# Performance work log

Hardware: AMD Instinct MI355X
Metric: run time of the kernel (lower is better)

The kernel has to match this reference:

```python
import jax, jax.numpy as jnp
import numpy as np

EPS = 1.0 / 137.0  # fine-structure-constant epsilon used throughout the Yat ops


def yat_dense(x, W, b, alpha):
    # x: [..., C], W: [C, F] -> [..., F]
    dot = jnp.einsum('btc,cf->btf', x, W)
    x_norm = jnp.sum(x * x, axis=-1, keepdims=True)        # [..., 1]
    w_norm = jnp.sum(W * W, axis=0)                         # [F]
    dist = x_norm + w_norm - 2.0 * dot
    y = dot * dot / (dist + EPS)
    y = y + b
    F = W.shape[1]
    scale = (np.sqrt(F) / np.log(1.0 + F)) ** 1.0           # base; alpha exponent applied below
    return y * ((np.float32(np.sqrt(F)) / np.float32(np.log1p(F))) ** alpha)


def setup_inputs() -> dict:
    key = jax.random.key(0)
    ks = jax.random.split(key, 8)
    B, T, C = 4, 1024, 768
    x = jax.random.normal(ks[0], (B, T, C), dtype=jnp.float32)
    mask = jnp.tril(jnp.ones((T, T), dtype=bool))[None, None, :, :]  # causal [1,1,T,T]
    sd = 1.0 / np.sqrt(C)
    W_attn = jax.random.normal(ks[1], (C, 3 * C), dtype=jnp.float32) * sd
    b_attn = jnp.zeros((3 * C,), dtype=jnp.float32)
    alpha_attn = jnp.ones((), dtype=jnp.float32)
    W_proj = jax.random.normal(ks[2], (C, C), dtype=jnp.float32) * sd
    b_proj = jnp.zeros((C,), dtype=jnp.float32)
    alpha_proj = jnp.ones((), dtype=jnp.float32)
    return {"x": x, "mask": mask, "W_attn": W_attn, "b_attn": b_attn,
            "alpha_attn": alpha_attn, "W_proj": W_proj, "b_proj": b_proj,
            "alpha_proj": alpha_proj}


def reference(x, mask, W_attn, b_attn, alpha_attn, W_proj, b_proj, alpha_proj):
    B, T, C = x.shape
    H = 12
    D = C // H  # head_dim
    qkv = yat_dense(x, W_attn, b_attn, alpha_attn)          # [B,T,3C]
    qkv = qkv.reshape(B, T, 3 * H, D)
    q, k, v = jnp.array_split(qkv, 3, axis=2)
    q = jnp.transpose(q, (0, 2, 1, 3))                       # [B,H,T,D]
    k = jnp.transpose(k, (0, 2, 1, 3))
    v = jnp.transpose(v, (0, 2, 1, 3))
    scale = 1.0 / np.float32(np.sqrt(D))
    dot = jnp.einsum('bhid,bhjd->bhij', q, k)                # [B,H,T,T]
    sq_dot = jnp.square(dot * scale)
    q_norm = jnp.sum(jnp.square(q), axis=-1)[..., None]      # [B,H,T,1]
    k_norm = jnp.sum(jnp.square(k), axis=-1)[..., None, :]   # [B,H,1,T]
    sq_dist = q_norm + k_norm - 2.0 * dot * scale
    attn = sq_dot / (sq_dist + EPS)
    attn = jnp.where(mask, attn, jnp.finfo(jnp.float32).min)
    attn = jax.nn.softmax(attn, axis=-1)
    out = jnp.einsum('bhij,bhjd->bhid', attn, v)             # [B,H,T,D]
    out = jnp.transpose(out, (0, 2, 1, 3)).reshape(B, T, C)
    out = yat_dense(out, W_proj, b_proj, alpha_proj)         # [B,T,C]
    return out
```

## Files before the change

kernel.cpp:

```cpp
#include <hip/hip_runtime.h>
#include <math.h>

#define EPS_YAT (1.0f/137.0f)

typedef unsigned short u16;
typedef unsigned int u32;
typedef __attribute__((ext_vector_type(8))) __bf16 bf16x8;
typedef __attribute__((ext_vector_type(4))) float f32x4;

__device__ __forceinline__ float4 ld4(const float* p) { return *(const float4*)p; }

__device__ __forceinline__ u16 bf16_rne(float f) {
    u32 u = __float_as_uint(f);
    u32 r = (u + 0x7fffu + ((u >> 16) & 1u)) >> 16;
    return (u16)r;
}
__device__ __forceinline__ float bf16_f(u16 h) {
    return __uint_as_float(((u32)h) << 16);
}

__device__ __forceinline__ void glds16(const u16* g, u16* s) {
    __builtin_amdgcn_global_load_lds(
        (const __attribute__((address_space(1))) void*)g,
        (__attribute__((address_space(3))) void*)s,
        16, 0, 0);
}

__global__ void colnorm_part2(const float* __restrict__ Wa, const float* __restrict__ Wp,
                              float* __restrict__ pa, float* __restrict__ pp) {
    __shared__ float sm[256];
    const float* W; float* part; int N, colbase;
    if (blockIdx.x < 36) { W = Wa; part = pa; N = 2304; colbase = blockIdx.x * 64; }
    else                 { W = Wp; part = pp; N = 768;  colbase = (blockIdx.x - 36) * 64; }
    const int col = colbase + (threadIdx.x & 63);
    const int q = threadIdx.x >> 6;
    const int k0 = blockIdx.y * 48 + q * 12;
    float s = 0.f;
    for (int k = k0; k < k0 + 12; ++k) {
        float w = W[(size_t)k * N + col];
        s += w * w;
    }
    sm[threadIdx.x] = s;
    __syncthreads();
    if (threadIdx.x < 64)
        part[(size_t)blockIdx.y * N + col] =
            sm[threadIdx.x] + sm[threadIdx.x + 64] + sm[threadIdx.x + 128] + sm[threadIdx.x + 192];
}

__global__ void colnorm_reduce2(const float* __restrict__ pa, const float* __restrict__ pp,
                                float* __restrict__ wa, float* __restrict__ wp,
                                float* __restrict__ an_zero) {
    int gid = blockIdx.x * 256 + threadIdx.x;
    if (gid < 2304) {
        float s = 0.f;
        #pragma unroll
        for (int i = 0; i < 16; ++i) s += pa[(size_t)i * 2304 + gid];
        wa[gid] = s;
    } else if (gid < 3072) {
        int g = gid - 2304;
        float s = 0.f;
        #pragma unroll
        for (int i = 0; i < 16; ++i) s += pp[(size_t)i * 768 + g];
        wp[g] = s;
    }
    int z = gid - 3072;
    if (z >= 0 && z < 4096) an_zero[z] = 0.f;
}

__global__ void split_rownorm(const float* __restrict__ X, u16* __restrict__ Xh,
                              u16* __restrict__ Xl, float* __restrict__ rn) {
    int wave = threadIdx.x >> 6;
    int lane = threadIdx.x & 63;
    int row = blockIdx.x * 4 + wave;
    const float* xr = X + (size_t)row * 768;
    u16* xh = Xh + (size_t)row * 768;
    u16* xl = Xl + (size_t)row * 768;
    float s = 0.f;
    #pragma unroll
    for (int k = lane * 4; k < 768; k += 256) {
        float4 v = ld4(xr + k);
        s += v.x * v.x + v.y * v.y + v.z * v.z + v.w * v.w;
        u16 h0 = bf16_rne(v.x), h1 = bf16_rne(v.y), h2 = bf16_rne(v.z), h3 = bf16_rne(v.w);
        u16 l0 = bf16_rne(v.x - bf16_f(h0));
        u16 l1 = bf16_rne(v.y - bf16_f(h1));
        u16 l2 = bf16_rne(v.z - bf16_f(h2));
        u16 l3 = bf16_rne(v.w - bf16_f(h3));
        uint2 hp, lp;
        hp.x = (u32)h0 | ((u32)h1 << 16); hp.y = (u32)h2 | ((u32)h3 << 16);
        lp.x = (u32)l0 | ((u32)l1 << 16); lp.y = (u32)l2 | ((u32)l3 << 16);
        *(uint2*)(xh + k) = hp;
        *(uint2*)(xl + k) = lp;
    }
    for (int off = 32; off; off >>= 1) s += __shfl_down(s, off);
    if (lane == 0) rn[row] = s;
}

__global__ void split_wt_kernel(const float* __restrict__ W, u16* __restrict__ Th,
                                u16* __restrict__ Tl, int K, int N) {
    __shared__ float tile[64 * 68];
    const int tid = threadIdx.x;
    const int n0 = blockIdx.x << 6;
    const int k0 = blockIdx.y << 6;
    const int rr = tid >> 4;
    const int cc = (tid & 15) << 2;
    #pragma unroll
    for (int s = 0; s < 4; ++s) {
        int k_l = rr + s * 16;
        *(float4*)&tile[k_l * 68 + cc] = ld4(W + (size_t)(k0 + k_l) * N + n0 + cc);
    }
    __syncthreads();
    #pragma unroll
    for (int s = 0; s < 4; ++s) {
        int n_l = rr + s * 16;
        float a0 = tile[(cc + 0) * 68 + n_l];
        float a1 = tile[(cc + 1) * 68 + n_l];
        float a2 = tile[(cc + 2) * 68 + n_l];
        float a3 = tile[(cc + 3) * 68 + n_l];
        u16 h0 = bf16_rne(a0), h1 = bf16_rne(a1), h2 = bf16_rne(a2), h3 = bf16_rne(a3);
        u16 l0 = bf16_rne(a0 - bf16_f(h0));
        u16 l1 = bf16_rne(a1 - bf16_f(h1));
        u16 l2 = bf16_rne(a2 - bf16_f(h2));
        u16 l3 = bf16_rne(a3 - bf16_f(h3));
        uint2 hp, lp;
        hp.x = (u32)h0 | ((u32)h1 << 16); hp.y = (u32)h2 | ((u32)h3 << 16);
        lp.x = (u32)l0 | ((u32)l1 << 16); lp.y = (u32)l2 | ((u32)l3 << 16);
        size_t o = (size_t)(n0 + n_l) * K + k0 + cc;
        *(uint2*)(Th + o) = hp;
        *(uint2*)(Tl + o) = lp;
    }
}

template<int SPLIT, int BIG>
__global__ __launch_bounds__(256, BIG ? 2 : 4)
void yat_gemm_mfma(const u16* __restrict__ Ah, const u16* __restrict__ Al,
                   const u16* __restrict__ Bh, const u16* __restrict__ Bl,
                   const float* __restrict__ bias, const float* __restrict__ xn,
                   const float* __restrict__ wnc, const float* __restrict__ alphap,
                   const float Fdim, float* __restrict__ out,
                   u16* __restrict__ outh, u16* __restrict__ outl,
                   float* __restrict__ qn, float* __restrict__ kn,
                   const int N, const int K) {
    constexpr int TM = BIG ? 128 : 64;
    constexpr int TN = BIG ? 128 : 64;
    constexpr int JN = BIG ? 4 : 1;
    __shared__ __align__(16) u16 lds[(TM + TN) * 64 * 2];
    const int tid = threadIdx.x;
    const int nwg = gridDim.x * gridDim.y;
    const int orig = blockIdx.y * gridDim.x + blockIdx.x;
    const int swz = (orig & 7) * (nwg >> 3) + (orig >> 3);
    const int m0 = (swz / gridDim.x) * TM;
    const int n0 = (swz % gridDim.x) * TN;
    const int w = tid >> 6;
    const int l = tid & 63;
    const int lm = l & 15;
    const int kq = l >> 4;
    const int kq4 = kq << 2;
    const int WM = BIG ? ((w >> 1) << 6) : 0;
    const int WN = BIG ? ((w & 1) << 6) : (w << 4);

    const int lrow = l >> 3;
    const int lchunk = (l & 7) << 3;

    u16* sAh = lds;
    u16* sAl = lds + TM * 64;
    u16* sBh = lds + 2 * TM * 64;
    u16* sBl = lds + 2 * TM * 64 + TN * 64;

    f32x4 acc[4][JN] = {};

    for (int k0 = 0; k0 < K; k0 += 64) {
        __syncthreads();
        #pragma unroll
        for (int c = 0; c < TM / 32; ++c) {
            const int r0w = (TM / 4) * w + 8 * c;
            const size_t go = (size_t)(m0 + r0w + lrow) * K + k0 + lchunk;
            glds16(Ah + go, sAh + r0w * 64);
            glds16(Al + go, sAl + r0w * 64);
        }
        #pragma unroll
        for (int c = 0; c < TN / 32; ++c) {
            const int r0w = (TN / 4) * w + 8 * c;
            const size_t go = (size_t)(n0 + r0w + lrow) * K + k0 + lchunk;
            glds16(Bh + go, sBh + r0w * 64);
            glds16(Bl + go, sBl + r0w * 64);
        }
        __syncthreads();

        #pragma unroll
        for (int kk = 0; kk < 2; ++kk) {
            bf16x8 fah[4], fal[4], fbh[JN], fbl[JN];
            #pragma unroll
            for (int i = 0; i < 4; ++i) {
                const int ra = (WM + i * 16 + lm) * 64 + kk * 32 + (kq << 3);
                fah[i] = *(const bf16x8*)&sAh[ra];
                fal[i] = *(const bf16x8*)&sAl[ra];
            }
            #pragma unroll
            for (int j = 0; j < JN; ++j) {
                const int rb = (WN + j * 16 + lm) * 64 + kk * 32 + (kq << 3);
                fbh[j] = *(const bf16x8*)&sBh[rb];
                fbl[j] = *(const bf16x8*)&sBl[rb];
            }
            #pragma unroll
            for (int i = 0; i < 4; ++i)
                #pragma unroll
                for (int j = 0; j < JN; ++j) {
                    f32x4 c = acc[i][j];
                    c = __builtin_amdgcn_mfma_f32_16x16x32_bf16(fah[i], fbh[j], c, 0, 0, 0);
                    c = __builtin_amdgcn_mfma_f32_16x16x32_bf16(fah[i], fbl[j], c, 0, 0, 0);
                    c = __builtin_amdgcn_mfma_f32_16x16x32_bf16(fal[i], fbh[j], c, 0, 0, 0);
                    acc[i][j] = c;
                }
        }
    }

    const float scale = powf(sqrtf(Fdim) / log1pf(Fdim), *alphap);
    float pp[4][4];
    #pragma unroll
    for (int i = 0; i < 4; ++i) {
        const int mbase = m0 + WM + i * 16 + kq4;
        #pragma unroll
        for (int r = 0; r < 4; ++r) pp[i][r] = 0.f;
        #pragma unroll
        for (int j = 0; j < JN; ++j) {
            const int n = n0 + WN + j * 16 + lm;
            const float w2 = wnc[n];
            const float bv = bias[n];
            #pragma unroll
            for (int r = 0; r < 4; ++r) {
                const int m = mbase + r;
                float d = acc[i][j][r];
                float den = xn[m] + w2 - 2.f * d + EPS_YAT;
                float v = (d * d / den + bv) * scale;
                if constexpr (SPLIT) {
                    u16 hh = bf16_rne(v);
                    outh[(size_t)m * N + n] = hh;
                    outl[(size_t)m * N + n] = bf16_rne(v - bf16_f(hh));
                    pp[i][r] += v * v;
                } else {
                    out[(size_t)m * N + n] = v;
                }
            }
        }
    }

    if constexpr (SPLIT) {
        const int hcol = n0 + WN;
        if (hcol < 1536) {
            #pragma unroll
            for (int i = 0; i < 4; ++i)
                #pragma unroll
                for (int r = 0; r < 4; ++r) {
                    float s = pp[i][r];
                    s += __shfl_xor(s, 1, 16);
                    s += __shfl_xor(s, 2, 16);
                    s += __shfl_xor(s, 4, 16);
                    s += __shfl_xor(s, 8, 16);
                    if (lm == 0) {
                        const int m = m0 + WM + i * 16 + kq4 + r;
                        const int bb = m >> 10, t = m & 1023;
                        if (hcol < 768)
                            qn[(bb * 12 + (hcol >> 6)) * 1024 + t] = s;
                        else
                            kn[(bb * 12 + ((hcol - 768) >> 6)) * 1024 + t] = s;
                    }
                }
        }
    }
}

#define MFMA_B16(a, b, c) __builtin_amdgcn_mfma_f32_16x16x32_bf16(a, b, c, 0, 0, 0)

#define ST_TILE(j) { \
    const int kro = ((j)*16 + lm) * 72 + (kq << 3); \
    bf16x8 kh = *(const bf16x8*)&KPh[kro]; \
    bf16x8 kl = *(const bf16x8*)&KPl[kro]; \
    st##j = MFMA_B16(kh, qh0, st##j); \
    st##j = MFMA_B16(kl, qh0, st##j); \
    st##j = MFMA_B16(kh, ql0, st##j); \
    kh = *(const bf16x8*)&KPh[kro + 32]; \
    kl = *(const bf16x8*)&KPl[kro + 32]; \
    st##j = MFMA_B16(kh, qh1, st##j); \
    st##j = MFMA_B16(kl, qh1, st##j); \
    st##j = MFMA_B16(kh, ql1, st##j); \
}

#define YAT_EL(j, r) { \
    float sv = st##j[r] * 0.125f; \
    float den = qnm + kns[(j)*16 + kq4 + (r)] - 2.f * sv + EPS_YAT; \
    float v = sv * sv / den; \
    if (diag && ((j)*16 + kq4 + (r) > wband + lm)) v = -3e38f; \
    st##j[r] = v; mm = fmaxf(mm, v); }
#define YAT_TILE(j) YAT_EL(j,0) YAT_EL(j,1) YAT_EL(j,2) YAT_EL(j,3)

#define PEXP_TILE(j) { \
    float p0 = __expf(st##j[0] - mnew), p1 = __expf(st##j[1] - mnew); \
    float p2 = __expf(st##j[2] - mnew), p3 = __expf(st##j[3] - mnew); \
    rs += p0 + p1 + p2 + p3; \
    u16 h0 = bf16_rne(p0), h1 = bf16_rne(p1), h2 = bf16_rne(p2), h3 = bf16_rne(p3); \
    uint2 hp; hp.x = (u32)h0 | ((u32)h1 << 16); hp.y = (u32)h2 | ((u32)h3 << 16); \
    *(uint2*)&KPh[pmrow + (j)*16 + kq4] = hp; \
    u16 e0 = bf16_rne(p0 - bf16_f(h0)), e1 = bf16_rne(p1 - bf16_f(h1)); \
    u16 e2 = bf16_rne(p2 - bf16_f(h2)), e3 = bf16_rne(p3 - bf16_f(h3)); \
    uint2 lp; lp.x = (u32)e0 | ((u32)e1 << 16); lp.y = (u32)e2 | ((u32)e3 << 16); \
    *(uint2*)&KPl[pmrow + (j)*16 + kq4] = lp; }

#define PV_TILE(j) { \
    const int vro = ((j)*16 + lm) * 72 + vkq8; \
    bf16x8 vh = *(const bf16x8*)&Vth[vro]; \
    bf16x8 vl = *(const bf16x8*)&Vtl[vro]; \
    ac##j = MFMA_B16(ph0, vh, ac##j); \
    ac##j = MFMA_B16(pl0, vh, ac##j); \
    ac##j = MFMA_B16(ph0, vl, ac##j); \
    vh = *(const bf16x8*)&Vth[vro + 32]; \
    vl = *(const bf16x8*)&Vtl[vro + 32]; \
    ac##j = MFMA_B16(ph1, vh, ac##j); \
    ac##j = MFMA_B16(pl1, vh, ac##j); \
    ac##j = MFMA_B16(ph1, vl, ac##j); \
}

#define WRVT(dst, v2, m) { \
    dst[(sj * 4 + 16 * (m) + 0) * 72 + toks] = (u16)((v2).x); \
    dst[(sj * 4 + 16 * (m) + 1) * 72 + toks] = (u16)((v2).x >> 16); \
    dst[(sj * 4 + 16 * (m) + 2) * 72 + toks] = (u16)((v2).y); \
    dst[(sj * 4 + 16 * (m) + 3) * 72 + toks] = (u16)((v2).y >> 16); }

__global__ __launch_bounds__(256, 2)
void yat_flash_mfma(const u16* __restrict__ qh_g, const u16* __restrict__ ql_g,
                    const float* __restrict__ qn, const float* __restrict__ kn,
                    u16* __restrict__ outh, u16* __restrict__ outl,
                    float* __restrict__ an_g) {
    __shared__ __align__(16) u16 KPh[64 * 72], KPl[64 * 72];
    __shared__ __align__(16) u16 Vth[64 * 72], Vtl[64 * 72];
    __shared__ float kns[64];

    const int tid = threadIdx.x;
    const int L = blockIdx.x;
    const int u = L / 48;
    const int qt = (u & 1) ? (u >> 1) : (15 - (u >> 1));
    const int bh = L % 48;
    const int h = bh % 12, b = bh / 12;
    const int wave = tid >> 6;
    const int lane = tid & 63;
    const int lm = lane & 15;
    const int kq = lane >> 4;
    const int kq4 = kq << 2;
    const int wband = wave << 4;
    const int sr = tid >> 2;
    const int sj = tid & 3;
    const int toks = sr ^ (sj << 3);
    const int vkq8 = (kq ^ (lm >> 2)) << 3;
    const size_t base = (size_t)(b * 1024) * 2304 + h * 64;

    {
        const size_t qoff = base + (size_t)((qt << 6) + sr) * 2304 + sj * 16;
        *(uint4*)&KPh[sr * 72 + sj * 16]     = *(const uint4*)(qh_g + qoff);
        *(uint4*)&KPh[sr * 72 + sj * 16 + 8] = *(const uint4*)(qh_g + qoff + 8);
        *(uint4*)&KPl[sr * 72 + sj * 16]     = *(const uint4*)(ql_g + qoff);
        *(uint4*)&KPl[sr * 72 + sj * 16 + 8] = *(const uint4*)(ql_g + qoff + 8);
    }
    const float qnm = qn[bh * 1024 + (qt << 6) + wband + lm];

    const size_t r0 = base + (size_t)sr * 2304;
    uint4 kh0 = *(const uint4*)(qh_g + r0 + 768 + sj * 16);
    uint4 kh1 = *(const uint4*)(qh_g + r0 + 768 + sj * 16 + 8);
    uint4 kl0 = *(const uint4*)(ql_g + r0 + 768 + sj * 16);
    uint4 kl1 = *(const uint4*)(ql_g + r0 + 768 + sj * 16 + 8);
    uint2 vh0 = *(const uint2*)(qh_g + r0 + 1536 + sj * 4);
    uint2 vh1 = *(const uint2*)(qh_g + r0 + 1536 + sj * 4 + 16);
    uint2 vh2 = *(const uint2*)(qh_g + r0 + 1536 + sj * 4 + 32);
    uint2 vh3 = *(const uint2*)(qh_g + r0 + 1536 + sj * 4 + 48);
    uint2 vl0 = *(const uint2*)(ql_g + r0 + 1536 + sj * 4);
    uint2 vl1 = *(const uint2*)(ql_g + r0 + 1536 + sj * 4 + 16);
    uint2 vl2 = *(const uint2*)(ql_g + r0 + 1536 + sj * 4 + 32);
    uint2 vl3 = *(const uint2*)(ql_g + r0 + 1536 + sj * 4 + 48);
    float knS = (tid < 64) ? kn[bh * 1024 + tid] : 0.f;

    __syncthreads();

    const int qrow = (wband + lm) * 72;
    const bf16x8 qh0 = *(const bf16x8*)&KPh[qrow + (kq << 3)];
    const bf16x8 qh1 = *(const bf16x8*)&KPh[qrow + 32 + (kq << 3)];
    const bf16x8 ql0 = *(const bf16x8*)&KPl[qrow + (kq << 3)];
    const bf16x8 ql1 = *(const bf16x8*)&KPl[qrow + 32 + (kq << 3)];

    f32x4 ac0 = {}, ac1 = {}, ac2 = {}, ac3 = {};
    float mrun = -3e38f, lrun = 0.f;
    const int pmrow = (wband + lm) * 72;

    for (int kt = 0; kt <= qt; ++kt) {
        __syncthreads();
        *(uint4*)&KPh[sr * 72 + sj * 16]     = kh0;
        *(uint4*)&KPh[sr * 72 + sj * 16 + 8] = kh1;
        *(uint4*)&KPl[sr * 72 + sj * 16]     = kl0;
        *(uint4*)&KPl[sr * 72 + sj * 16 + 8] = kl1;
        WRVT(Vth, vh0, 0) WRVT(Vth, vh1, 1) WRVT(Vth, vh2, 2) WRVT(Vth, vh3, 3)
        WRVT(Vtl, vl0, 0) WRVT(Vtl, vl1, 1) WRVT(Vtl, vl2, 2) WRVT(Vtl, vl3, 3)
        if (tid < 64) kns[tid] = knS;
        __syncthreads();

        if (kt < qt) {
            const size_t r = base + (size_t)(((kt + 1) << 6) + sr) * 2304;
            kh0 = *(const uint4*)(qh_g + r + 768 + sj * 16);
            kh1 = *(const uint4*)(qh_g + r + 768 + sj * 16 + 8);
            kl0 = *(const uint4*)(ql_g + r + 768 + sj * 16);
            kl1 = *(const uint4*)(ql_g + r + 768 + sj * 16 + 8);
            vh0 = *(const uint2*)(qh_g + r + 1536 + sj * 4);
            vh1 = *(const uint2*)(qh_g + r + 1536 + sj * 4 + 16);
            vh2 = *(const uint2*)(qh_g + r + 1536 + sj * 4 + 32);
            vh3 = *(const uint2*)(qh_g + r + 1536 + sj * 4 + 48);
            vl0 = *(const uint2*)(ql_g + r + 1536 + sj * 4);
            vl1 = *(const uint2*)(ql_g + r + 1536 + sj * 4 + 16);
            vl2 = *(const uint2*)(ql_g + r + 1536 + sj * 4 + 32);
            vl3 = *(const uint2*)(ql_g + r + 1536 + sj * 4 + 48);
            if (tid < 64) knS = kn[bh * 1024 + ((kt + 1) << 6) + tid];
        }

        f32x4 st0 = {}, st1 = {}, st2 = {}, st3 = {};
        __builtin_amdgcn_s_setprio(1);
        ST_TILE(0) ST_TILE(1) ST_TILE(2) ST_TILE(3)
        __builtin_amdgcn_s_setprio(0);
        __syncthreads();

        const bool diag = (kt == qt);
        float mm = -3e38f;
        YAT_TILE(0) YAT_TILE(1) YAT_TILE(2) YAT_TILE(3)
        mm = fmaxf(mm, __shfl_xor(mm, 16));
        mm = fmaxf(mm, __shfl_xor(mm, 32));
        const float mnew = fmaxf(mrun, mm);
        if (!__all(mm <= mrun)) {
            const float al = __expf(mrun - mnew);
            const float a0 = __shfl(al, kq4 + 0, 16);
            const float a1 = __shfl(al, kq4 + 1, 16);
            const float a2 = __shfl(al, kq4 + 2, 16);
            const float a3 = __shfl(al, kq4 + 3, 16);
            ac0[0] *= a0; ac0[1] *= a1; ac0[2] *= a2; ac0[3] *= a3;
            ac1[0] *= a0; ac1[1] *= a1; ac1[2] *= a2; ac1[3] *= a3;
            ac2[0] *= a0; ac2[1] *= a1; ac2[2] *= a2; ac2[3] *= a3;
            ac3[0] *= a0; ac3[1] *= a1; ac3[2] *= a2; ac3[3] *= a3;
            lrun *= al;
        }
        mrun = mnew;
        float rs = 0.f;
        PEXP_TILE(0) PEXP_TILE(1) PEXP_TILE(2) PEXP_TILE(3)
        rs += __shfl_xor(rs, 16);
        rs += __shfl_xor(rs, 32);
        lrun += rs;
        __syncthreads();

        const bf16x8 ph0 = *(const bf16x8*)&KPh[pmrow + (kq << 3)];
        const bf16x8 ph1 = *(const bf16x8*)&KPh[pmrow + 32 + (kq << 3)];
        const bf16x8 pl0 = *(const bf16x8*)&KPl[pmrow + (kq << 3)];
        const bf16x8 pl1 = *(const bf16x8*)&KPl[pmrow + 32 + (kq << 3)];
        __builtin_amdgcn_s_setprio(1);
        PV_TILE(0) PV_TILE(1) PV_TILE(2) PV_TILE(3)
        __builtin_amdgcn_s_setprio(0);
    }

    const float i0 = 1.f / __shfl(lrun, kq4 + 0, 16);
    const float i1 = 1.f / __shfl(lrun, kq4 + 1, 16);
    const float i2 = 1.f / __shfl(lrun, kq4 + 2, 16);
    const float i3 = 1.f / __shfl(lrun, kq4 + 3, 16);
    const size_t obase = (size_t)(b * 1024 + (qt << 6) + wband + kq4) * 768 + h * 64 + lm;
    u16* oph = outh + obase;
    u16* opl = outl + obase;
    float rsum0 = 0.f, rsum1 = 0.f, rsum2 = 0.f, rsum3 = 0.f;
    #define STORE_E(j, r, iv) { \
        float ov = ac##j[r] * iv; \
        rsum##r += ov * ov; \
        u16 hh = bf16_rne(ov); \
        oph[(size_t)(r) * 768 + (j)*16] = hh; \
        opl[(size_t)(r) * 768 + (j)*16] = bf16_rne(ov - bf16_f(hh)); }
    #define STORE_T(j) { STORE_E(j,0,i0) STORE_E(j,1,i1) STORE_E(j,2,i2) STORE_E(j,3,i3) }
    STORE_T(0) STORE_T(1) STORE_T(2) STORE_T(3)
    #undef STORE_T
    #undef STORE_E
    const int arow = b * 1024 + (qt << 6) + wband + kq4;
    #define REDROW(r) { \
        float s = rsum##r; \
        s += __shfl_xor(s, 1, 16); \
        s += __shfl_xor(s, 2, 16); \
        s += __shfl_xor(s, 4, 16); \
        s += __shfl_xor(s, 8, 16); \
        if (lm == 0) atomicAdd(&an_g[arow + (r)], s); }
    REDROW(0) REDROW(1) REDROW(2) REDROW(3)
    #undef REDROW
}

extern "C" void kernel_launch(void* const* d_in, const int* in_sizes, int n_in,
                              void* d_out, int out_size, void* d_ws, size_t ws_size,
                              hipStream_t stream) {
    const float* x          = (const float*)d_in[0];
    const float* W_attn     = (const float*)d_in[2];
    const float* b_attn     = (const float*)d_in[3];
    const float* alpha_attn = (const float*)d_in[4];
    const float* W_proj     = (const float*)d_in[5];
    const float* b_proj     = (const float*)d_in[6];
    const float* alpha_proj = (const float*)d_in[7];

    float* ws       = (float*)d_ws;
    u16*   qkvh     = (u16*)ws;
    u16*   qkvl     = (u16*)(ws + 4718592);
    float* xn       = ws + 12582912;
    float* an       = ws + 12587008;
    float* wn_attn  = ws + 12591104;
    float* wn_proj  = ws + 12593408;
    float* qn       = ws + 12594176;
    float* kn       = ws + 12643328;

    float* cn_part_a = ws + 9437184;
    float* cn_part_p = ws + 9437184 + 36864;
    u16* xh  = (u16*)(ws + 9437184);
    u16* xl  = (u16*)(ws + 11010048);
    u16* aoh = (u16*)(ws + 9437184);
    u16* aol = (u16*)(ws + 11010048);
    u16* wth = (u16*)d_out;
    u16* wtl = (u16*)d_out + 1769472;
    u16* wph = (u16*)(ws + 3145728);
    u16* wpl = (u16*)(ws + 3440640);

    colnorm_part2<<<dim3(48, 16), 256, 0, stream>>>(W_attn, W_proj, cn_part_a, cn_part_p);
    colnorm_reduce2<<<28, 256, 0, stream>>>(cn_part_a, cn_part_p, wn_attn, wn_proj, an);
    split_rownorm<<<1024, 256, 0, stream>>>(x, xh, xl, xn);
    split_wt_kernel<<<dim3(36, 12), 256, 0, stream>>>(W_attn, wth, wtl, 768, 2304);
    yat_gemm_mfma<1, 1><<<dim3(18, 32), 256, 0, stream>>>(
        xh, xl, wth, wtl, b_attn, xn, wn_attn, alpha_attn, 2304.f,
        nullptr, qkvh, qkvl, qn, kn, 2304, 768);
    yat_flash_mfma<<<768, 256, 0, stream>>>(qkvh, qkvl, qn, kn, aoh, aol, an);
    split_wt_kernel<<<dim3(12, 12), 256, 0, stream>>>(W_proj, wph, wpl, 768, 768);
    yat_gemm_mfma<0, 0><<<dim3(12, 64), 256, 0, stream>>>(
        aoh, aol, wph, wpl, b_proj, an, wn_proj, alpha_proj, 768.f,
        (float*)d_out, nullptr, nullptr, nullptr, nullptr, 768, 768);
}
```

Before: 252.0 us.

## Double-buffer GEMM LDS tiles with async prefetch and XOR-swizzled layout

Restructures the split-bf16 MFMA GEMM main loop to use two LDS buffers with a K-step of 32. The next tile is prefetched via global_load_lds while the current one is consumed, with explicit vmcnt waits in place of full syncthreads. The LDS layout also gains an XOR swizzle on 16-byte chunks to reduce bank conflicts on fragment reads. In exchange there are twice as many loop iterations with barriers, and the hand-tuned vmcnt counts are fragile if the number of loads per stage changes.

```diff
diff --git a/kernel.cpp b/kernel.cpp
--- a/kernel.cpp
+++ b/kernel.cpp
@@ -143,7 +143,10 @@
     constexpr int TM = BIG ? 128 : 64;
     constexpr int TN = BIG ? 128 : 64;
     constexpr int JN = BIG ? 4 : 1;
-    __shared__ __align__(16) u16 lds[(TM + TN) * 64 * 2];
+    constexpr int ASZ = TM * 32;
+    constexpr int BSZ = TN * 32;
+    constexpr int BUF = 2 * ASZ + 2 * BSZ;
+    __shared__ __align__(16) u16 lds[2 * BUF];
     const int tid = threadIdx.x;
     const int nwg = gridDim.x * gridDim.y;
     const int orig = blockIdx.y * gridDim.x + blockIdx.x;
@@ -158,61 +161,74 @@
     const int WM = BIG ? ((w >> 1) << 6) : 0;
     const int WN = BIG ? ((w & 1) << 6) : (w << 4);
 
-    const int lrow = l >> 3;
-    const int lchunk = (l & 7) << 3;
-
-    u16* sAh = lds;
-    u16* sAl = lds + TM * 64;
-    u16* sBh = lds + 2 * TM * 64;
-    u16* sBl = lds + 2 * TM * 64 + TN * 64;
+    const int lrow = l >> 2;
+    const int swch = ((l & 3) ^ (lrow & 3)) << 3;
 
     f32x4 acc[4][JN] = {};
 
-    for (int k0 = 0; k0 < K; k0 += 64) {
-        __syncthreads();
-        #pragma unroll
-        for (int c = 0; c < TM / 32; ++c) {
-            const int r0w = (TM / 4) * w + 8 * c;
-            const size_t go = (size_t)(m0 + r0w + lrow) * K + k0 + lchunk;
-            glds16(Ah + go, sAh + r0w * 64);
-            glds16(Al + go, sAl + r0w * 64);
-        }
-        #pragma unroll
-        for (int c = 0; c < TN / 32; ++c) {
-            const int r0w = (TN / 4) * w + 8 * c;
-            const size_t go = (size_t)(n0 + r0w + lrow) * K + k0 + lchunk;
-            glds16(Bh + go, sBh + r0w * 64);
-            glds16(Bl + go, sBl + r0w * 64);
-        }
-        __syncthreads();
-
-        #pragma unroll
-        for (int kk = 0; kk < 2; ++kk) {
-            bf16x8 fah[4], fal[4], fbh[JN], fbl[JN];
-            #pragma unroll
-            for (int i = 0; i < 4; ++i) {
-                const int ra = (WM + i * 16 + lm) * 64 + kk * 32 + (kq << 3);
-                fah[i] = *(const bf16x8*)&sAh[ra];
-                fal[i] = *(const bf16x8*)&sAl[ra];
-            }
+    #define STAGE(bufp, kk) { \
+        u16* sb = lds + (bufp) * BUF; \
+        _Pragma("unroll") \
+        for (int c = 0; c < TM / 64; ++c) { \
+            const int rg = 16 * (4 * c + w); \
+            const size_t go = (size_t)(m0 + rg + lrow) * K + (kk) + swch; \
+            glds16(Ah + go, sb + rg * 32); \
+            glds16(Al + go, sb + ASZ + rg * 32); \
+        } \
+        _Pragma("unroll") \
+        for (int c = 0; c < TN / 64; ++c) { \
+            const int rg = 16 * (4 * c + w); \
+            const size_t go = (size_t)(n0 + rg + lrow) * K + (kk) + swch; \
+            glds16(Bh + go, sb + 2 * ASZ + rg * 32); \
+            glds16(Bl + go, sb + 2 * ASZ + BSZ + rg * 32); \
+        } }
+
+    STAGE(0, 0);
+    int cur = 0;
+    for (int k0 = 0; k0 < K; k0 += 32) {
+        __builtin_amdgcn_s_barrier();
+        if (k0 + 32 < K) {
+            STAGE(cur ^ 1, k0 + 32);
+            if constexpr (BIG) asm volatile("s_waitcnt vmcnt(8)" ::: "memory");
+            else               asm volatile("s_waitcnt vmcnt(4)" ::: "memory");
+        } else {
+            asm volatile("s_waitcnt vmcnt(0)" ::: "memory");
+        }
+        __builtin_amdgcn_sched_barrier(0);
+        __builtin_amdgcn_s_barrier();
+
+        const u16* sb  = lds + cur * BUF;
+        const u16* sAh = sb;
+        const u16* sAl = sb + ASZ;
+        const u16* sBh = sb + 2 * ASZ;
+        const u16* sBl = sb + 2 * ASZ + BSZ;
+        const int ch = ((kq ^ (lm & 3)) << 3);
+        bf16x8 fah[4], fal[4], fbh[JN], fbl[JN];
+        #pragma unroll
+        for (int i = 0; i < 4; ++i) {
+            const int ra = (WM + i * 16 + lm) * 32 + ch;
+            fah[i] = *(const bf16x8*)&sAh[ra];
+            fal[i] = *(const bf16x8*)&sAl[ra];
+        }
+        #pragma unroll
+        for (int j = 0; j < JN; ++j) {
+            const int rb = (WN + j * 16 + lm) * 32 + ch;
+            fbh[j] = *(const bf16x8*)&sBh[rb];
+            fbl[j] = *(const bf16x8*)&sBl[rb];
+        }
+        #pragma unroll
+        for (int i = 0; i < 4; ++i)
             #pragma unroll
             for (int j = 0; j < JN; ++j) {
-                const int rb = (WN + j * 16 + lm) * 64 + kk * 32 + (kq << 3);
-                fbh[j] = *(const bf16x8*)&sBh[rb];
-                fbl[j] = *(const bf16x8*)&sBl[rb];
+                f32x4 c = acc[i][j];
+                c = __builtin_amdgcn_mfma_f32_16x16x32_bf16(fah[i], fbh[j], c, 0, 0, 0);
+                c = __builtin_amdgcn_mfma_f32_16x16x32_bf16(fah[i], fbl[j], c, 0, 0, 0);
+                c = __builtin_amdgcn_mfma_f32_16x16x32_bf16(fal[i], fbh[j], c, 0, 0, 0);
+                acc[i][j] = c;
             }
-            #pragma unroll
-            for (int i = 0; i < 4; ++i)
-                #pragma unroll
-                for (int j = 0; j < JN; ++j) {
-                    f32x4 c = acc[i][j];
-                    c = __builtin_amdgcn_mfma_f32_16x16x32_bf16(fah[i], fbh[j], c, 0, 0, 0);
-                    c = __builtin_amdgcn_mfma_f32_16x16x32_bf16(fah[i], fbl[j], c, 0, 0, 0);
-                    c = __builtin_amdgcn_mfma_f32_16x16x32_bf16(fal[i], fbh[j], c, 0, 0, 0);
-                    acc[i][j] = c;
-                }
-        }
-    }
+        cur ^= 1;
+    }
+    #undef STAGE
 
     const float scale = powf(sqrtf(Fdim) / log1pf(Fdim), *alphap);
     float pp[4][4];
```

Result: faster. 245.1 us (-2.8%).
